# Performance work log

Measured on AMD Instinct MI355X. Metric: run time of the kernel, lower is better.

The kernel has to match this reference:

```python
import jax, jax.numpy as jnp
import numpy as np

B, C, H, W = 16, 512, 64, 64
C1 = C // (C // 256)  # 256: conv output channels, per scale = in_dim // 256


def setup_inputs() -> dict:
    key = jax.random.key(0)
    k1, k2, k3, k4 = jax.random.split(key, 4)
    x = jax.random.normal(k1, (B, C, H, W), dtype=jnp.float32)
    # 1x1 conv params (kaiming-ish scale for C fan-in)
    conv_w = jax.random.normal(k2, (C1, C, 1, 1), dtype=jnp.float32) * (1.0 / np.sqrt(C))
    conv_b = jax.random.normal(k3, (C1,), dtype=jnp.float32) * 0.01
    # gamma is nn.Parameter(zeros(1)) in torch; use a random value so the
    # attention branch actually contributes to the output under test.
    gamma = jax.random.normal(k4, (1,), dtype=jnp.float32)
    return {"x": x, "conv_w": conv_w, "conv_b": conv_b, "gamma": gamma}


def reference(x, conv_w, conv_b, gamma):
    b, c, h, w = x.shape
    hw = h * w
    # 1x1 conv == channel-mixing matmul
    proj_query = jnp.einsum('bchw,oc->bohw', x, conv_w[:, :, 0, 0]) + conv_b[None, :, None, None]
    xres = proj_query                     # residual (B, C1, H, W)
    c1 = proj_query.shape[1]
    q = proj_query.reshape(b, c1, hw)     # (B, C1, HW)
    k = x.reshape(b, c, hw)               # (B, C,  HW)
    # einsum 'ijk,iklm->ijlm' over (B,HW,8,C/8) then view back == q @ k^T
    energy = jnp.einsum('bqn,bcn->bqc', q, k) / jnp.asarray(np.sqrt(hw), x.dtype)
    attention = jax.nn.softmax(energy, axis=-1)   # (B, C1, C), softmax over C
    out = jnp.einsum('bqc,bcn->bqn', attention, k).reshape(b, c1, h, w)
    return gamma * out + xres
```

## Files before the change

### kernel.cpp

```cpp
#include <hip/hip_runtime.h>
#include <stdint.h>

#define B_  16
#define C_  512
#define C1_ 256
#define HW_ 4096

using bf16x8 = __attribute__((ext_vector_type(8))) short;
using f32x4  = __attribute__((ext_vector_type(4))) float;

__device__ __forceinline__ short f2bf(float f) {
  union { float f; unsigned int u; } v; v.f = f;
  unsigned int r = v.u + 0x7fffu + ((v.u >> 16) & 1u);
  return (short)(r >> 16);
}
__device__ __forceinline__ float bf2f(short s) {
  union { unsigned int u; float f; } v;
  v.u = ((unsigned int)(unsigned short)s) << 16;
  return v.f;
}

__device__ __forceinline__ void gload_lds16(const void* g, void* l) {
  __builtin_amdgcn_global_load_lds(
      (const __attribute__((address_space(1))) void*)g,
      (__attribute__((address_space(3))) void*)l, 16, 0, 0);
}

__global__ __launch_bounds__(256) void k_convert(const float* __restrict__ x,
                                                 short* __restrict__ Xbf,
                                                 short* __restrict__ XbfT) {
  __shared__ short T[128][72];
  const int n0 = blockIdx.x * 128, c0 = blockIdx.y * 64, b = blockIdx.z;
  const int t = threadIdx.x;
  const int i = t >> 2;
  const int jc = t & 3;
  const float* xrow = x + ((size_t)(b * C_ + c0 + i)) * HW_ + n0;
  short* yrow = Xbf + ((size_t)(b * C_ + c0 + i)) * HW_ + n0;
#pragma unroll
  for (int l = 0; l < 8; ++l) {
    const int n = 4 * jc + 16 * l;
    const float4 v = *(const float4*)(xrow + n);
    short4 o;
    o.x = f2bf(v.x); o.y = f2bf(v.y); o.z = f2bf(v.z); o.w = f2bf(v.w);
    *(short4*)(yrow + n) = o;
    T[n + 0][i] = o.x; T[n + 1][i] = o.y;
    T[n + 2][i] = o.z; T[n + 3][i] = o.w;
  }
  __syncthreads();
  const int nr = t & 127, ch = (t >> 7) * 32;
  short* orow = XbfT + ((size_t)b * HW_ + n0 + nr) * C_ + c0 + ch;
  const bf16x8 u0 = *(const bf16x8*)&T[nr][ch + 0];
  const bf16x8 u1 = *(const bf16x8*)&T[nr][ch + 8];
  const bf16x8 u2 = *(const bf16x8*)&T[nr][ch + 16];
  const bf16x8 u3 = *(const bf16x8*)&T[nr][ch + 24];
  *(bf16x8*)(orow + 0)  = u0;
  *(bf16x8*)(orow + 8)  = u1;
  *(bf16x8*)(orow + 16) = u2;
  *(bf16x8*)(orow + 24) = u3;
}

__global__ __launch_bounds__(256) void k_wconv(const float* __restrict__ W,
                                               short* __restrict__ Wbf) {
  const int q = blockIdx.x, t = threadIdx.x;
  const float2 v = ((const float2*)(W + (size_t)q * C_))[t];
  short2 o; o.x = f2bf(v.x); o.y = f2bf(v.y);
  ((short2*)(Wbf + (size_t)q * C_))[t] = o;
}

__global__ __launch_bounds__(256, 2) void k_q(const short* __restrict__ Wbf,
                                              const short* __restrict__ XbfT,
                                              const float* __restrict__ convb,
                                              short* __restrict__ Qbf) {
  __shared__ short As[128 * 32];
  __shared__ short Bs[128 * 32];
  const int t = threadIdx.x;
  const int mt = blockIdx.x & 1, nt = blockIdx.x >> 1, b = blockIdx.y;
  const short* Ab = Wbf + (size_t)(mt * 128) * C_;
  const short* Bb = XbfT + ((size_t)b * HW_ + nt * 128) * C_;
  const int lane = t & 63, w = t >> 6;
  const int wr = w >> 1, wc = w & 1;
  const int fr = lane & 15, fk = (lane >> 4) * 8;
  const int row_st = t >> 2, k_st = (t & 3) * 8;
  f32x4 acc[4][4] = {};
  for (int kk = 0; kk < 16; ++kk) {
    const int k0 = kk * 32 + k_st;
    gload_lds16(Ab + (size_t)row_st * C_ + k0, &As[t * 8]);
    gload_lds16(Ab + (size_t)(row_st + 64) * C_ + k0, &As[2048 + t * 8]);
    gload_lds16(Bb + (size_t)row_st * C_ + k0, &Bs[t * 8]);
    gload_lds16(Bb + (size_t)(row_st + 64) * C_ + k0, &Bs[2048 + t * 8]);
    __syncthreads();
    bf16x8 a[4], bv[4];
#pragma unroll
    for (int m = 0; m < 4; ++m)
      a[m] = *(const bf16x8*)&As[(wr * 64 + m * 16 + fr) * 32 + fk];
#pragma unroll
    for (int n = 0; n < 4; ++n)
      bv[n] = *(const bf16x8*)&Bs[(wc * 64 + n * 16 + fr) * 32 + fk];
#pragma unroll
    for (int m = 0; m < 4; ++m)
#pragma unroll
      for (int n = 0; n < 4; ++n)
        acc[m][n] = __builtin_amdgcn_mfma_f32_16x16x32_bf16(a[m], bv[n], acc[m][n], 0, 0, 0);
    __syncthreads();
  }
  const int q_base = mt * 128 + wr * 64;
  const int n_base = nt * 128 + wc * 64;
#pragma unroll
  for (int m = 0; m < 4; ++m)
#pragma unroll
    for (int n = 0; n < 4; ++n) {
      const int q = q_base + m * 16 + (lane >> 4) * 4;
      const int nn = n_base + n * 16 + (lane & 15);
#pragma unroll
      for (int r = 0; r < 4; ++r)
        Qbf[((size_t)b * C1_ + q + r) * HW_ + nn] = f2bf(acc[m][n][r] + convb[q + r]);
    }
}

__global__ __launch_bounds__(256, 2) void k_e(const short* __restrict__ Qbf,
                                              const short* __restrict__ Xbf,
                                              short* __restrict__ Ep) {
  __shared__ short As[128 * 32];
  __shared__ short Bs[128 * 32];
  const int t = threadIdx.x;
  const int b = blockIdx.x;
  const int qt = blockIdx.y & 1, ct = blockIdx.y >> 1;
  const int ks = blockIdx.z;
  const short* Ab = Qbf + ((size_t)b * C1_ + qt * 128) * HW_ + ks * 1024;
  const short* Bb = Xbf + ((size_t)b * C_ + ct * 128) * HW_ + ks * 1024;
  const int lane = t & 63, w = t >> 6;
  const int wr = w >> 1, wc = w & 1;
  const int fr = lane & 15, fk = (lane >> 4) * 8;
  const int row_st = t >> 2, k_st = (t & 3) * 8;
  f32x4 acc[4][4] = {};
  for (int kk = 0; kk < 32; ++kk) {
    const int k0 = kk * 32 + k_st;
    gload_lds16(Ab + (size_t)row_st * HW_ + k0, &As[t * 8]);
    gload_lds16(Ab + (size_t)(row_st + 64) * HW_ + k0, &As[2048 + t * 8]);
    gload_lds16(Bb + (size_t)row_st * HW_ + k0, &Bs[t * 8]);
    gload_lds16(Bb + (size_t)(row_st + 64) * HW_ + k0, &Bs[2048 + t * 8]);
    __syncthreads();
    bf16x8 a[4], bv[4];
#pragma unroll
    for (int m = 0; m < 4; ++m)
      a[m] = *(const bf16x8*)&As[(wr * 64 + m * 16 + fr) * 32 + fk];
#pragma unroll
    for (int n = 0; n < 4; ++n)
      bv[n] = *(const bf16x8*)&Bs[(wc * 64 + n * 16 + fr) * 32 + fk];
#pragma unroll
    for (int m = 0; m < 4; ++m)
#pragma unroll
      for (int n = 0; n < 4; ++n)
        acc[m][n] = __builtin_amdgcn_mfma_f32_16x16x32_bf16(a[m], bv[n], acc[m][n], 0, 0, 0);
    __syncthreads();
  }
  const int q_base = qt * 128 + wr * 64;
  const int c_base = ct * 128 + wc * 64;
#pragma unroll
  for (int m = 0; m < 4; ++m)
#pragma unroll
    for (int n = 0; n < 4; ++n) {
      const int q = q_base + m * 16 + (lane >> 4) * 4;
      const int c = c_base + n * 16 + (lane & 15);
#pragma unroll
      for (int r = 0; r < 4; ++r)
        Ep[(((size_t)ks * B_ + b) * C1_ + q + r) * C_ + c] = f2bf(acc[m][n][r]);
    }
}

__global__ __launch_bounds__(128) void k_softmax(const short* __restrict__ Ep,
                                                 const float* __restrict__ W,
                                                 const float* __restrict__ gamma,
                                                 short* __restrict__ Mb) {
  const int bq = blockIdx.x;
  const int b = bq >> 8, q = bq & 255;
  const int t = threadIdx.x;
  const float g = gamma[0];
  float e[4] = {0.f, 0.f, 0.f, 0.f};
#pragma unroll
  for (int ks = 0; ks < 4; ++ks) {
    const short4 v = *(const short4*)&Ep[(((size_t)ks * B_ + b) * C1_ + q) * C_ + t * 4];
    e[0] += bf2f(v.x); e[1] += bf2f(v.y); e[2] += bf2f(v.z); e[3] += bf2f(v.w);
  }
#pragma unroll
  for (int d = 0; d < 4; ++d) e[d] *= 0.015625f;
  float mx = fmaxf(fmaxf(e[0], e[1]), fmaxf(e[2], e[3]));
#pragma unroll
  for (int off = 1; off < 64; off <<= 1) mx = fmaxf(mx, __shfl_xor(mx, off));
  __shared__ float red[2];
  if ((t & 63) == 0) red[t >> 6] = mx;
  __syncthreads();
  mx = fmaxf(red[0], red[1]);
  const float e0 = __expf(e[0] - mx), e1 = __expf(e[1] - mx);
  const float e2 = __expf(e[2] - mx), e3 = __expf(e[3] - mx);
  float sum = (e0 + e1) + (e2 + e3);
#pragma unroll
  for (int off = 1; off < 64; off <<= 1) sum += __shfl_xor(sum, off);
  __shared__ float red2[2];
  if ((t & 63) == 0) red2[t >> 6] = sum;
  __syncthreads();
  const float inv = 1.0f / (red2[0] + red2[1]);
  const float4 wv = ((const float4*)(W + (size_t)q * C_))[t];
  short4 o;
  o.x = f2bf(g * e0 * inv + wv.x);
  o.y = f2bf(g * e1 * inv + wv.y);
  o.z = f2bf(g * e2 * inv + wv.z);
  o.w = f2bf(g * e3 * inv + wv.w);
  ((short4*)(Mb + (size_t)bq * C_))[t] = o;
}

__global__ __launch_bounds__(256, 2) void k_out(const short* __restrict__ Mb,
                                                const short* __restrict__ XbfT,
                                                const float* __restrict__ convb,
                                                float* __restrict__ out) {
  __shared__ short As[128 * 32];
  __shared__ short Bs[128 * 32];
  const int t = threadIdx.x;
  const int mt = blockIdx.x & 1, nt = blockIdx.x >> 1, b = blockIdx.y;
  const short* Ab = Mb + ((size_t)b * C1_ + mt * 128) * C_;
  const short* Bb = XbfT + ((size_t)b * HW_ + nt * 128) * C_;
  const int lane = t & 63, w = t >> 6;
  const int wr = w >> 1, wc = w & 1;
  const int fr = lane & 15, fk = (lane >> 4) * 8;
  const int row_st = t >> 2, k_st = (t & 3) * 8;
  f32x4 acc[4][4] = {};
  for (int kk = 0; kk < 16; ++kk) {
    const int k0 = kk * 32 + k_st;
    gload_lds16(Ab + (size_t)row_st * C_ + k0, &As[t * 8]);
    gload_lds16(Ab + (size_t)(row_st + 64) * C_ + k0, &As[2048 + t * 8]);
    gload_lds16(Bb + (size_t)row_st * C_ + k0, &Bs[t * 8]);
    gload_lds16(Bb + (size_t)(row_st + 64) * C_ + k0, &Bs[2048 + t * 8]);
    __syncthreads();
    bf16x8 a[4], bv[4];
#pragma unroll
    for (int m = 0; m < 4; ++m)
      a[m] = *(const bf16x8*)&As[(wr * 64 + m * 16 + fr) * 32 + fk];
#pragma unroll
    for (int n = 0; n < 4; ++n)
      bv[n] = *(const bf16x8*)&Bs[(wc * 64 + n * 16 + fr) * 32 + fk];
#pragma unroll
    for (int m = 0; m < 4; ++m)
#pragma unroll
      for (int n = 0; n < 4; ++n)
        acc[m][n] = __builtin_amdgcn_mfma_f32_16x16x32_bf16(a[m], bv[n], acc[m][n], 0, 0, 0);
    __syncthreads();
  }
  const int o_base = mt * 128 + wr * 64;
  const int n_base = nt * 128 + wc * 64;
#pragma unroll
  for (int m = 0; m < 4; ++m)
#pragma unroll
    for (int n = 0; n < 4; ++n) {
      const int oo = o_base + m * 16 + (lane >> 4) * 4;
      const int nn = n_base + n * 16 + (lane & 15);
#pragma unroll
      for (int r = 0; r < 4; ++r)
        out[((size_t)b * C1_ + oo + r) * HW_ + nn] = acc[m][n][r] + convb[oo + r];
    }
}

extern "C" void kernel_launch(void* const* d_in, const int* in_sizes, int n_in,
                              void* d_out, int out_size, void* d_ws, size_t ws_size,
                              hipStream_t stream) {
  const float* x      = (const float*)d_in[0];
  const float* conv_w = (const float*)d_in[1];
  const float* conv_b = (const float*)d_in[2];
  const float* gamma  = (const float*)d_in[3];
  float* out = (float*)d_out;

  char* ws = (char*)d_ws;
  short* Xbf  = (short*)(ws);
  short* XbfT = (short*)(ws + 67108864);
  short* Qbf  = (short*)(ws + 134217728);
  short* Mb   = (short*)(ws + 134217728);
  short* Ep   = (short*)(ws + 167772160);
  short* Wbf  = (short*)(ws + 184549376);

  k_convert<<<dim3(32, 8, 16), 256, 0, stream>>>(x, Xbf, XbfT);
  k_wconv<<<256, 256, 0, stream>>>(conv_w, Wbf);
  k_q<<<dim3(64, 16), 256, 0, stream>>>(Wbf, XbfT, conv_b, Qbf);
  k_e<<<dim3(16, 8, 4), 256, 0, stream>>>(Qbf, Xbf, Ep);
  k_softmax<<<4096, 128, 0, stream>>>(Ep, conv_w, gamma, Mb);
  k_out<<<dim3(64, 16), 256, 0, stream>>>(Mb, XbfT, conv_b, out);
}
```

Measured before the change: 173.7 us.

## Double-buffer GEMM LDS stages, swizzle transpose, and deepen split-K for energy

The three MFMA GEMMs now share a templated loop that double-buffers the LDS tiles, issuing the next k-slice's global-to-LDS loads before computing the current one and using one barrier per iteration instead of two. The convert kernel writes 16-byte vectors into an XOR-swizzled LDS tile, so the transposed read-back avoids bank conflicts and writes two rows per thread. When the workspace is large enough, the energy GEMM splits K eight ways instead of four to get more blocks, which costs more partial-sum traffic in the softmax. LDS use doubles, which may limit occupancy.

```diff
diff --git a/kernel.cpp b/kernel.cpp
--- a/kernel.cpp
+++ b/kernel.cpp
@@ -29,34 +29,43 @@
 __global__ __launch_bounds__(256) void k_convert(const float* __restrict__ x,
                                                  short* __restrict__ Xbf,
                                                  short* __restrict__ XbfT) {
-  __shared__ short T[128][72];
+  __shared__ short T2[64 * 144];
   const int n0 = blockIdx.x * 128, c0 = blockIdx.y * 64, b = blockIdx.z;
   const int t = threadIdx.x;
   const int i = t >> 2;
   const int jc = t & 3;
   const float* xrow = x + ((size_t)(b * C_ + c0 + i)) * HW_ + n0;
   short* yrow = Xbf + ((size_t)(b * C_ + c0 + i)) * HW_ + n0;
-#pragma unroll
-  for (int l = 0; l < 8; ++l) {
-    const int n = 4 * jc + 16 * l;
-    const float4 v = *(const float4*)(xrow + n);
-    short4 o;
-    o.x = f2bf(v.x); o.y = f2bf(v.y); o.z = f2bf(v.z); o.w = f2bf(v.w);
-    *(short4*)(yrow + n) = o;
-    T[n + 0][i] = o.x; T[n + 1][i] = o.y;
-    T[n + 2][i] = o.z; T[n + 3][i] = o.w;
+  const int gx = i >> 3;
+#pragma unroll
+  for (int l = 0; l < 4; ++l) {
+    const int n = jc * 8 + l * 32;
+    const float4 v0 = *(const float4*)(xrow + n);
+    const float4 v1 = *(const float4*)(xrow + n + 4);
+    bf16x8 o;
+    o[0] = f2bf(v0.x); o[1] = f2bf(v0.y); o[2] = f2bf(v0.z); o[3] = f2bf(v0.w);
+    o[4] = f2bf(v1.x); o[5] = f2bf(v1.y); o[6] = f2bf(v1.z); o[7] = f2bf(v1.w);
+    *(bf16x8*)(yrow + n) = o;
+    *(bf16x8*)&T2[i * 144 + ((((n >> 3) ^ gx) << 3))] = o;
   }
   __syncthreads();
-  const int nr = t & 127, ch = (t >> 7) * 32;
-  short* orow = XbfT + ((size_t)b * HW_ + n0 + nr) * C_ + c0 + ch;
-  const bf16x8 u0 = *(const bf16x8*)&T[nr][ch + 0];
-  const bf16x8 u1 = *(const bf16x8*)&T[nr][ch + 8];
-  const bf16x8 u2 = *(const bf16x8*)&T[nr][ch + 16];
-  const bf16x8 u3 = *(const bf16x8*)&T[nr][ch + 24];
-  *(bf16x8*)(orow + 0)  = u0;
-  *(bf16x8*)(orow + 8)  = u1;
-  *(bf16x8*)(orow + 16) = u2;
-  *(bf16x8*)(orow + 24) = u3;
+  const int cb = (t & 7) * 8;
+  const int r0 = (t >> 3) * 2;
+#pragma unroll
+  for (int p = 0; p < 2; ++p) {
+    const int r = r0 + p * 64;
+    bf16x8 oa, ob;
+#pragma unroll
+    for (int e = 0; e < 8; ++e) {
+      const int c = cb + e;
+      const int idx = c * 144 + (((((r >> 3) ^ (c >> 3))) << 3) | (r & 7));
+      const short2 pr = *(const short2*)&T2[idx];
+      oa[e] = pr.x; ob[e] = pr.y;
+    }
+    short* orow = XbfT + ((size_t)b * HW_ + n0 + r) * C_ + c0 + cb;
+    *(bf16x8*)(orow)      = oa;
+    *(bf16x8*)(orow + C_) = ob;
+  }
 }
 
 __global__ __launch_bounds__(256) void k_wconv(const float* __restrict__ W,
@@ -67,42 +76,68 @@
   ((short2*)(Wbf + (size_t)q * C_))[t] = o;
 }
 
+template<int KITER, int LDK>
+__device__ __forceinline__ void nt_loop(const short* __restrict__ Ab,
+                                        const short* __restrict__ Bb,
+                                        short* As, short* Bs, int t,
+                                        f32x4 (&acc)[4][4]) {
+  const int lane = t & 63, w = t >> 6;
+  const int wr = w >> 1, wc = w & 1;
+  const int fr = lane & 15, fk = (lane >> 4) * 8;
+  const int row_st = t >> 2, k_st = (t & 3) * 8;
+
+#define STAGE_(buf, kk)                                                         \
+  {                                                                             \
+    const int k0_ = (kk) * 32 + k_st;                                           \
+    gload_lds16(Ab + (size_t)row_st * LDK + k0_, As + (buf) * 4096 + t * 8);    \
+    gload_lds16(Ab + (size_t)(row_st + 64) * LDK + k0_,                         \
+                As + (buf) * 4096 + 2048 + t * 8);                              \
+    gload_lds16(Bb + (size_t)row_st * LDK + k0_, Bs + (buf) * 4096 + t * 8);    \
+    gload_lds16(Bb + (size_t)(row_st + 64) * LDK + k0_,                         \
+                Bs + (buf) * 4096 + 2048 + t * 8);                              \
+  }
+
+  STAGE_(0, 0);
+  asm volatile("s_waitcnt vmcnt(0)" ::: "memory");
+  __builtin_amdgcn_s_barrier();
+  int cur = 0;
+  for (int kk = 0; kk < KITER; ++kk) {
+    if (kk + 1 < KITER) STAGE_(cur ^ 1, kk + 1);
+    const short* Ac = As + cur * 4096;
+    const short* Bc = Bs + cur * 4096;
+    bf16x8 a[4], bv[4];
+#pragma unroll
+    for (int m = 0; m < 4; ++m)
+      a[m] = *(const bf16x8*)&Ac[(wr * 64 + m * 16 + fr) * 32 + fk];
+#pragma unroll
+    for (int n = 0; n < 4; ++n)
+      bv[n] = *(const bf16x8*)&Bc[(wc * 64 + n * 16 + fr) * 32 + fk];
+#pragma unroll
+    for (int m = 0; m < 4; ++m)
+#pragma unroll
+      for (int n = 0; n < 4; ++n)
+        acc[m][n] = __builtin_amdgcn_mfma_f32_16x16x32_bf16(a[m], bv[n], acc[m][n], 0, 0, 0);
+    asm volatile("s_waitcnt vmcnt(0)" ::: "memory");
+    __builtin_amdgcn_s_barrier();
+    cur ^= 1;
+  }
+#undef STAGE_
+}
+
 __global__ __launch_bounds__(256, 2) void k_q(const short* __restrict__ Wbf,
                                               const short* __restrict__ XbfT,
                                               const float* __restrict__ convb,
                                               short* __restrict__ Qbf) {
-  __shared__ short As[128 * 32];
-  __shared__ short Bs[128 * 32];
+  __shared__ short As[2 * 4096];
+  __shared__ short Bs[2 * 4096];
   const int t = threadIdx.x;
   const int mt = blockIdx.x & 1, nt = blockIdx.x >> 1, b = blockIdx.y;
   const short* Ab = Wbf + (size_t)(mt * 128) * C_;
   const short* Bb = XbfT + ((size_t)b * HW_ + nt * 128) * C_;
-  const int lane = t & 63, w = t >> 6;
-  const int wr = w >> 1, wc = w & 1;
-  const int fr = lane & 15, fk = (lane >> 4) * 8;
-  const int row_st = t >> 2, k_st = (t & 3) * 8;
   f32x4 acc[4][4] = {};
-  for (int kk = 0; kk < 16; ++kk) {
-    const int k0 = kk * 32 + k_st;
-    gload_lds16(Ab + (size_t)row_st * C_ + k0, &As[t * 8]);
-    gload_lds16(Ab + (size_t)(row_st + 64) * C_ + k0, &As[2048 + t * 8]);
-    gload_lds16(Bb + (size_t)row_st * C_ + k0, &Bs[t * 8]);
-    gload_lds16(Bb + (size_t)(row_st + 64) * C_ + k0, &Bs[2048 + t * 8]);
-    __syncthreads();
-    bf16x8 a[4], bv[4];
-#pragma unroll
-    for (int m = 0; m < 4; ++m)
-      a[m] = *(const bf16x8*)&As[(wr * 64 + m * 16 + fr) * 32 + fk];
-#pragma unroll
-    for (int n = 0; n < 4; ++n)
-      bv[n] = *(const bf16x8*)&Bs[(wc * 64 + n * 16 + fr) * 32 + fk];
-#pragma unroll
-    for (int m = 0; m < 4; ++m)
-#pragma unroll
-      for (int n = 0; n < 4; ++n)
-        acc[m][n] = __builtin_amdgcn_mfma_f32_16x16x32_bf16(a[m], bv[n], acc[m][n], 0, 0, 0);
-    __syncthreads();
-  }
+  nt_loop<16, C_>(Ab, Bb, As, Bs, t, acc);
+  const int lane = t & 63, w = t >> 6;
+  const int wr = w >> 1, wc = w & 1;
   const int q_base = mt * 128 + wr * 64;
   const int n_base = nt * 128 + wc * 64;
 #pragma unroll
@@ -117,43 +152,22 @@
     }
 }
 
+template<int KITER>
 __global__ __launch_bounds__(256, 2) void k_e(const short* __restrict__ Qbf,
                                               const short* __restrict__ Xbf,
                                               short* __restrict__ Ep) {
-  __shared__ short As[128 * 32];
-  __shared__ short Bs[128 * 32];
+  __shared__ short As[2 * 4096];
+  __shared__ short Bs[2 * 4096];
   const int t = threadIdx.x;
   const int b = blockIdx.x;
   const int qt = blockIdx.y & 1, ct = blockIdx.y >> 1;
   const int ks = blockIdx.z;
-  const short* Ab = Qbf + ((size_t)b * C1_ + qt * 128) * HW_ + ks * 1024;
-  const short* Bb = Xbf + ((size_t)b * C_ + ct * 128) * HW_ + ks * 1024;
-  const int lane = t & 63, w = t >> 6;
-  const int wr = w >> 1, wc = w & 1;
-  const int fr = lane & 15, fk = (lane >> 4) * 8;
-  const int row_st = t >> 2, k_st = (t & 3) * 8;
+  const short* Ab = Qbf + ((size_t)b * C1_ + qt * 128) * HW_ + (size_t)ks * (KITER * 32);
+  const short* Bb = Xbf + ((size_t)b * C_ + ct * 128) * HW_ + (size_t)ks * (KITER * 32);
   f32x4 acc[4][4] = {};
-  for (int kk = 0; kk < 32; ++kk) {
-    const int k0 = kk * 32 + k_st;
-    gload_lds16(Ab + (size_t)row_st * HW_ + k0, &As[t * 8]);
-    gload_lds16(Ab + (size_t)(row_st + 64) * HW_ + k0, &As[2048 + t * 8]);
-    gload_lds16(Bb + (size_t)row_st * HW_ + k0, &Bs[t * 8]);
-    gload_lds16(Bb + (size_t)(row_st + 64) * HW_ + k0, &Bs[2048 + t * 8]);
-    __syncthreads();
-    bf16x8 a[4], bv[4];
-#pragma unroll
-    for (int m = 0; m < 4; ++m)
-      a[m] = *(const bf16x8*)&As[(wr * 64 + m * 16 + fr) * 32 + fk];
-#pragma unroll
-    for (int n = 0; n < 4; ++n)
-      bv[n] = *(const bf16x8*)&Bs[(wc * 64 + n * 16 + fr) * 32 + fk];
-#pragma unroll
-    for (int m = 0; m < 4; ++m)
-#pragma unroll
-      for (int n = 0; n < 4; ++n)
-        acc[m][n] = __builtin_amdgcn_mfma_f32_16x16x32_bf16(a[m], bv[n], acc[m][n], 0, 0, 0);
-    __syncthreads();
-  }
+  nt_loop<KITER, HW_>(Ab, Bb, As, Bs, t, acc);
+  const int lane = t & 63, w = t >> 6;
+  const int wr = w >> 1, wc = w & 1;
   const int q_base = qt * 128 + wr * 64;
   const int c_base = ct * 128 + wc * 64;
 #pragma unroll
@@ -168,6 +182,7 @@
     }
 }
 
+template<int NKS>
 __global__ __launch_bounds__(128) void k_softmax(const short* __restrict__ Ep,
                                                  const float* __restrict__ W,
                                                  const float* __restrict__ gamma,
@@ -178,7 +193,7 @@
   const float g = gamma[0];
   float e[4] = {0.f, 0.f, 0.f, 0.f};
 #pragma unroll
-  for (int ks = 0; ks < 4; ++ks) {
+  for (int ks = 0; ks < NKS; ++ks) {
     const short4 v = *(const short4*)&Ep[(((size_t)ks * B_ + b) * C1_ + q) * C_ + t * 4];
     e[0] += bf2f(v.x); e[1] += bf2f(v.y); e[2] += bf2f(v.z); e[3] += bf2f(v.w);
   }
@@ -213,38 +228,16 @@
                                                 const short* __restrict__ XbfT,
                                                 const float* __restrict__ convb,
                                                 float* __restrict__ out) {
-  __shared__ short As[128 * 32];
-  __shared__ short Bs[128 * 32];
+  __shared__ short As[2 * 4096];
+  __shared__ short Bs[2 * 4096];
   const int t = threadIdx.x;
   const int mt = blockIdx.x & 1, nt = blockIdx.x >> 1, b = blockIdx.y;
   const short* Ab = Mb + ((size_t)b * C1_ + mt * 128) * C_;
   const short* Bb = XbfT + ((size_t)b * HW_ + nt * 128) * C_;
-  const int lane = t & 63, w = t >> 6;
-  const int wr = w >> 1, wc = w & 1;
-  const int fr = lane & 15, fk = (lane >> 4) * 8;
-  const int row_st = t >> 2, k_st = (t & 3) * 8;
   f32x4 acc[4][4] = {};
-  for (int kk = 0; kk < 16; ++kk) {
-    const int k0 = kk * 32 + k_st;
-    gload_lds16(Ab + (size_t)row_st * C_ + k0, &As[t * 8]);
-    gload_lds16(Ab + (size_t)(row_st + 64) * C_ + k0, &As[2048 + t * 8]);
-    gload_lds16(Bb + (size_t)row_st * C_ + k0, &Bs[t * 8]);
-    gload_lds16(Bb + (size_t)(row_st + 64) * C_ + k0, &Bs[2048 + t * 8]);
-    __syncthreads();
-    bf16x8 a[4], bv[4];
-#pragma unroll
-    for (int m = 0; m < 4; ++m)
-      a[m] = *(const bf16x8*)&As[(wr * 64 + m * 16 + fr) * 32 + fk];
-#pragma unroll
-    for (int n = 0; n < 4; ++n)
-      bv[n] = *(const bf16x8*)&Bs[(wc * 64 + n * 16 + fr) * 32 + fk];
-#pragma unroll
-    for (int m = 0; m < 4; ++m)
-#pragma unroll
-      for (int n = 0; n < 4; ++n)
-        acc[m][n] = __builtin_amdgcn_mfma_f32_16x16x32_bf16(a[m], bv[n], acc[m][n], 0, 0, 0);
-    __syncthreads();
-  }
+  nt_loop<16, C_>(Ab, Bb, As, Bs, t, acc);
+  const int lane = t & 63, w = t >> 6;
+  const int wr = w >> 1, wc = w & 1;
   const int o_base = mt * 128 + wr * 64;
   const int n_base = nt * 128 + wc * 64;
 #pragma unroll
@@ -274,12 +267,18 @@
   short* Qbf  = (short*)(ws + 134217728);
   short* Mb   = (short*)(ws + 134217728);
   short* Ep   = (short*)(ws + 167772160);
-  short* Wbf  = (short*)(ws + 184549376);
+  const bool big = ws_size >= 201588736ull;
+  short* Wbf  = (short*)(ws + (big ? 201326592u : 184549376u));
 
   k_convert<<<dim3(32, 8, 16), 256, 0, stream>>>(x, Xbf, XbfT);
   k_wconv<<<256, 256, 0, stream>>>(conv_w, Wbf);
   k_q<<<dim3(64, 16), 256, 0, stream>>>(Wbf, XbfT, conv_b, Qbf);
-  k_e<<<dim3(16, 8, 4), 256, 0, stream>>>(Qbf, Xbf, Ep);
-  k_softmax<<<4096, 128, 0, stream>>>(Ep, conv_w, gamma, Mb);
+  if (big) {
+    k_e<16><<<dim3(16, 8, 8), 256, 0, stream>>>(Qbf, Xbf, Ep);
+    k_softmax<8><<<4096, 128, 0, stream>>>(Ep, conv_w, gamma, Mb);
+  } else {
+    k_e<32><<<dim3(16, 8, 4), 256, 0, stream>>>(Qbf, Xbf, Ep);
+    k_softmax<4><<<4096, 128, 0, stream>>>(Ep, conv_w, gamma, Mb);
+  }
   k_out<<<dim3(64, 16), 256, 0, stream>>>(Mb, XbfT, conv_b, out);
 }
```

Measured after the change: 156.2 us. -10.1%, faster.
